# Kernel optimization log

Measured on AMD Instinct MI355X. Metric: run time of the kernel, lower is better.

## Reference

```python
import jax, jax.numpy as jnp
import numpy as np

EPS = 1e-6
SLIDING_WINDOW = 512
ROPE_BASE = 10000.0  # rope_local_base_freq for sliding_attention layers


def _rms_norm(x, w=None):
    # Gemma-style RMSNorm computed in fp32 then cast back
    xf = x.astype(jnp.float32)
    out = xf * jax.lax.rsqrt(jnp.mean(xf * xf, axis=-1, keepdims=True) + EPS)
    if w is not None:
        out = out * w.astype(jnp.float32)
    return out.astype(x.dtype)


def _rotate_half(x):
    x1, x2 = jnp.split(x, 2, axis=-1)
    return jnp.concatenate((-x2, x1), axis=-1)


def setup_inputs() -> dict:
    key = jax.random.key(0)
    ks = jax.random.split(key, 6)
    B, S, H, NH, NKV, D = 1, 4096, 2048, 8, 2, 256
    hidden_states = jax.random.normal(ks[0], (B, S, H), dtype=jnp.float32)
    w_q = jax.random.normal(ks[1], (H, NH * D), dtype=jnp.float32) * 0.02
    w_k = jax.random.normal(ks[2], (H, NKV * D), dtype=jnp.float32) * 0.02
    w_v = jax.random.normal(ks[3], (H, NKV * D), dtype=jnp.float32) * 0.02
    w_o = jax.random.normal(ks[4], (NH * D, H), dtype=jnp.float32) * 0.02
    q_norm_w = jnp.ones((D,), dtype=jnp.float32)
    k_norm_w = jnp.ones((D,), dtype=jnp.float32)
    # RoPE tables (local base freq, sliding layer)
    inv_freq = 1.0 / (ROPE_BASE ** (jnp.arange(0, D, 2, dtype=jnp.float32) / D))
    pos = jnp.arange(S, dtype=jnp.float32)
    freqs = pos[:, None] * inv_freq[None, :]          # [S, D/2]
    emb = jnp.concatenate((freqs, freqs), axis=-1)    # [S, D]
    cos = jnp.broadcast_to(jnp.cos(emb)[None], (B, S, D)).astype(jnp.float32)
    sin = jnp.broadcast_to(jnp.sin(emb)[None], (B, S, D)).astype(jnp.float32)
    return {"hidden_states": hidden_states, "w_q": w_q, "w_k": w_k, "w_v": w_v,
            "w_o": w_o, "q_norm_w": q_norm_w, "k_norm_w": k_norm_w,
            "cos": cos, "sin": sin}


def reference(hidden_states, w_q, w_k, w_v, w_o, q_norm_w, k_norm_w, cos, sin):
    B, S, _ = hidden_states.shape
    D = cos.shape[-1]
    NH = w_q.shape[1] // D
    NKV = w_k.shape[1] // D
    G = NH // NKV

    # projections -> [B, S, heads, D], per-head RMSNorm (Gemma3n-style)
    q = _rms_norm((hidden_states @ w_q).reshape(B, S, NH, D), q_norm_w)
    k = _rms_norm((hidden_states @ w_k).reshape(B, S, NKV, D), k_norm_w)
    v = _rms_norm((hidden_states @ w_v).reshape(B, S, NKV, D))  # v_norm: no scale

    q = q.transpose(0, 2, 1, 3)  # [B, NH, S, D]
    k = k.transpose(0, 2, 1, 3)  # [B, NKV, S, D]
    v = v.transpose(0, 2, 1, 3)

    # RoPE, cos/sin unsqueezed over the head dim
    c = cos[:, None, :, :]
    s = sin[:, None, :, :]
    q = q * c + _rotate_half(q) * s
    k = k * c + _rotate_half(k) * s

    # GQA: repeat KV heads
    k = jnp.repeat(k, G, axis=1)  # [B, NH, S, D]
    v = jnp.repeat(v, G, axis=1)

    # attention, scaling = 1.0 (q_norm replaces 1/sqrt(d) in this family)
    scores = jnp.einsum('bhqd,bhkd->bhqk', q, k)

    # causal + sliding-window mask
    i = jnp.arange(S)[:, None]
    j = jnp.arange(S)[None, :]
    mask = (j <= i) & ((i - j) < SLIDING_WINDOW)
    scores = jnp.where(mask[None, None], scores, jnp.finfo(scores.dtype).min)

    attn = jax.nn.softmax(scores.astype(jnp.float32), axis=-1).astype(q.dtype)
    out = jnp.einsum('bhqk,bhkd->bhqd', attn, v)
    out = out.transpose(0, 2, 1, 3).reshape(B, S, NH * D)
    return out @ w_o
```

## Files before the change

### kernel.cpp

```cpp
#include <hip/hip_runtime.h>
#include <hip/hip_bf16.h>

#define S_LEN 4096
#define HDIM  2048
#define NHQ   8
#define NKVH  2
#define DHEAD 256
#define WIN   512
#define NQKV  3072

typedef __hip_bfloat16 bf16_t;
using fragAB = __attribute__((ext_vector_type(8))) short;
using fragC  = __attribute__((ext_vector_type(4))) float;

struct __align__(8)  bf16x4 { bf16_t v[4]; };
struct __align__(16) bf16x8 { bf16_t v[8]; };

typedef unsigned int u32;
typedef const __attribute__((address_space(1))) u32* gas_ptr;
typedef __attribute__((address_space(3))) u32* las_ptr;

__device__ __forceinline__ void async_copy16(const void* g, void* l) {
  __builtin_amdgcn_global_load_lds((gas_ptr)g, (las_ptr)l, 16, 0, 0);
}

#define NEG_BIG (-3.0e38f)

__device__ __forceinline__ void split2(float x, bf16_t& hi, bf16_t& lo) {
  bf16_t h = __float2bfloat16(x);
  hi = h;
  lo = __float2bfloat16(x - (float)h);
}

__global__ __launch_bounds__(256) void prep0(
    const float* __restrict__ hid, bf16_t* __restrict__ hidh,
    bf16_t* __restrict__ hidl, const float* __restrict__ wq,
    const float* __restrict__ wk, const float* __restrict__ wv,
    bf16_t* __restrict__ hiT, bf16_t* __restrict__ loT) {
  __shared__ bf16_t th[32][33];
  __shared__ bf16_t tl[32][33];
  int bx = blockIdx.x;
  if (bx < 4096) {
    int i = (bx * 256 + threadIdx.x) * 8;
    float4 a = *(const float4*)(hid + i);
    float4 b = *(const float4*)(hid + i + 4);
    float xs[8] = {a.x, a.y, a.z, a.w, b.x, b.y, b.z, b.w};
    bf16x8 hv, lv;
#pragma unroll
    for (int j = 0; j < 8; ++j) split2(xs[j], hv.v[j], lv.v[j]);
    *(bf16x8*)(hidh + i) = hv;
    *(bf16x8*)(hidl + i) = lv;
  } else {
    int b2 = bx - 4096;
    int oc = (b2 % 96) * 32;
    int r0 = (b2 / 96) * 32;
    const float* src; int C, c0;
    if (oc < 2048)      { src = wq; C = 2048; c0 = oc; }
    else if (oc < 2560) { src = wk; C = 512;  c0 = oc - 2048; }
    else                { src = wv; C = 512;  c0 = oc - 2560; }
    int tx = threadIdx.x & 31, ty = threadIdx.x >> 5;
#pragma unroll
    for (int i = 0; i < 4; ++i) {
      float x = src[(size_t)(r0 + ty + i * 8) * C + c0 + tx];
      bf16_t h, l; split2(x, h, l);
      th[ty + i * 8][tx] = h;
      tl[ty + i * 8][tx] = l;
    }
    __syncthreads();
#pragma unroll
    for (int i = 0; i < 4; ++i) {
      hiT[(size_t)(oc + ty + i * 8) * HDIM + r0 + tx] = th[tx][ty + i * 8];
      loT[(size_t)(oc + ty + i * 8) * HDIM + r0 + tx] = tl[tx][ty + i * 8];
    }
  }
}

#define VMCNT_(n) asm volatile("s_waitcnt vmcnt(" #n ")" ::: "memory")
#define VMCNT(n) VMCNT_(n)
#define BARRIER()                     \
  {                                   \
    asm volatile("" ::: "memory");    \
    __builtin_amdgcn_s_barrier();     \
    asm volatile("" ::: "memory");    \
  }

#define MFMA_(a, b, c) __builtin_amdgcn_mfma_f32_16x16x32_bf16(a, b, c, 0, 0, 0)

#define OFF_AH 0
#define OFF_AL 16384
#define OFF_BH 32768
#define OFF_BL 45056
#define BUFSZ  57344

#define SPLIT_STEP()                                                    \
  {                                                                     \
    fragAB bh[4], bl[4];                                                \
    _Pragma("unroll") for (int j = 0; j < 4; ++j) {                     \
      const char* bp = bufc + (wn + j * 16 + l16) * 64 + rdq;           \
      bh[j] = *(const fragAB*)(bp + OFF_BH);                            \
      bl[j] = *(const fragAB*)(bp + OFF_BL);                            \
    }                                                                   \
    _Pragma("unroll") for (int p = 0; p < 2; ++p) {                     \
      fragAB ah[2], al[2];                                              \
      _Pragma("unroll") for (int u = 0; u < 2; ++u) {                   \
        const char* ap = bufc + (wm + (2 * p + u) * 16 + l16) * 64 + rdq;\
        ah[u] = *(const fragAB*)(ap + OFF_AH);                          \
        al[u] = *(const fragAB*)(ap + OFF_AL);                          \
      }                                                                 \
      __builtin_amdgcn_s_setprio(1);                                    \
      _Pragma("unroll") for (int j = 0; j < 4; ++j)                     \
        _Pragma("unroll") for (int u = 0; u < 2; ++u)                   \
          acc[2 * p + u][j] = MFMA_(al[u], bh[j], acc[2 * p + u][j]);   \
      _Pragma("unroll") for (int j = 0; j < 4; ++j)                     \
        _Pragma("unroll") for (int u = 0; u < 2; ++u)                   \
          acc[2 * p + u][j] = MFMA_(ah[u], bl[j], acc[2 * p + u][j]);   \
      _Pragma("unroll") for (int j = 0; j < 4; ++j)                     \
        _Pragma("unroll") for (int u = 0; u < 2; ++u)                   \
          acc[2 * p + u][j] = MFMA_(ah[u], bh[j], acc[2 * p + u][j]);   \
      __builtin_amdgcn_s_setprio(0);                                    \
    }                                                                   \
  }

__global__ __launch_bounds__(768, 3) void gemm_split2(
    const bf16_t* __restrict__ Ah, const bf16_t* __restrict__ Al,
    const bf16_t* __restrict__ Bh, const bf16_t* __restrict__ Bl,
    float* __restrict__ C, int M, int N, int K) {
  __shared__ __align__(16) char lds[2 * BUFSZ];
  const int t = threadIdx.x;
  const int wave = t >> 6, lane = t & 63;
  const int quad = lane >> 4, l16 = lane & 15;
  const int g = blockIdx.y * 16 + blockIdx.x;
  const int lby = (g & 7) * 2 + ((g >> 3) >> 4);
  const int lbx = (g >> 3) & 15;
  const int m0 = lby * 256, n0 = lbx * 192;
  const int wm = (wave / 3) * 64, wn = (wave % 3) * 64;
  const int rdq = (quad ^ ((l16 >> 1) & 3)) * 16;

  const size_t laneOff =
      (size_t)(lane >> 2) * K * 2 + 16 * ((lane & 3) ^ ((lane >> 3) & 3));

  const char* gbase[7];
  int ldsOff[7];
  if (wave < 8) {
#pragma unroll
    for (int pos = 0; pos < 3; ++pos) {
      int c = wave + 8 * pos;
      if (c < 12) {
        gbase[pos]  = (const char*)Bh + (size_t)(n0 + 16 * c) * K * 2;
        ldsOff[pos] = OFF_BH + c * 1024;
      } else {
        gbase[pos]  = (const char*)Bl + (size_t)(n0 + 16 * (c - 12)) * K * 2;
        ldsOff[pos] = OFF_BL + (c - 12) * 1024;
      }
    }
#pragma unroll
    for (int p = 0; p < 4; ++p) {
      int sub = wave & 3;
      int R0 = ((sub >> 1) & 1) * 128 + 32 * p + (sub & 1) * 16;
      const char* base = (const char*)(wave < 4 ? Ah : Al);
      gbase[3 + p]  = base + (size_t)(m0 + R0) * K * 2;
      ldsOff[3 + p] = (wave < 4 ? OFF_AH : OFF_AL) + R0 * 64;
    }
  }

  fragC zero4 = {0.f, 0.f, 0.f, 0.f};
  fragC acc[4][4];
#pragma unroll
  for (int i = 0; i < 4; ++i)
#pragma unroll
    for (int j = 0; j < 4; ++j) acc[i][j] = zero4;

  char* ldsc = (char*)lds;
  if (wave < 8) {
#pragma unroll
    for (int ps = 0; ps < 7; ++ps)
      async_copy16(gbase[ps] + laneOff, ldsc + ldsOff[ps]);
  }

  size_t kk = 64;
  int cur = 0;
  const int NS = K / 32;
  for (int it = 0; it < NS - 1; ++it) {
    const char* bufc = ldsc + cur * BUFSZ;
    char* nb = ldsc + (cur ^ 1) * BUFSZ;
    VMCNT(0); BARRIER();
    if (wave < 8) {
#pragma unroll
      for (int ps = 0; ps < 7; ++ps)
        async_copy16(gbase[ps] + kk + laneOff, nb + ldsOff[ps]);
    }
    kk += 64;
    SPLIT_STEP();
    cur ^= 1;
  }
  {
    const char* bufc = ldsc + cur * BUFSZ;
    VMCNT(0); BARRIER();
    SPLIT_STEP();
  }

#pragma unroll
  for (int i = 0; i < 4; ++i)
#pragma unroll
    for (int j = 0; j < 4; ++j)
#pragma unroll
      for (int r = 0; r < 4; ++r) {
        int row = m0 + wm + i * 16 + quad * 4 + r;
        int col = n0 + wn + j * 16 + l16;
        C[(size_t)row * N + col] = acc[i][j][r];
      }
}

#define BT_OFF_A 0
#define BT_OFF_B 32768
#define BT_BUFSZ 49152

struct ARegs2 { fragAB a[2][2]; };

__device__ __forceinline__ void lda_bt(ARegs2& r, const char* bufc, int wm,
                                       int p, int l16, int quad, int rx) {
#pragma unroll
  for (int u = 0; u < 2; ++u)
#pragma unroll
    for (int ks = 0; ks < 2; ++ks)
      r.a[u][ks] = *(const fragAB*)(bufc + BT_OFF_A +
                                    (wm + (2 * p + u) * 16 + l16) * 128 +
                                    (((ks * 4 + quad) ^ rx) * 16));
}

__device__ __forceinline__ void mfma_bt(fragC (&acc)[8][2], const ARegs2& r,
                                        const fragAB (&b)[2][2], int p) {
  __builtin_amdgcn_s_setprio(1);
#pragma unroll
  for (int ks = 0; ks < 2; ++ks)
#pragma unroll
    for (int j = 0; j < 2; ++j) {
      acc[2 * p][j]     = MFMA_(r.a[0][ks], b[j][ks], acc[2 * p][j]);
      acc[2 * p + 1][j] = MFMA_(r.a[1][ks], b[j][ks], acc[2 * p + 1][j]);
    }
  __builtin_amdgcn_s_setprio(0);
}

#define BT_LOADB()                                                        \
  _Pragma("unroll")                                                       \
  for (int j = 0; j < 2; ++j)                                             \
  _Pragma("unroll")                                                       \
    for (int ks = 0; ks < 2; ++ks)                                        \
      bfr[j][ks] = *(const fragAB*)(bufc + BT_OFF_B +                     \
                                    (wn + j * 16 + l16) * 128 +           \
                                    (((ks * 4 + quad) ^ rx) * 16));

#define BT_STEP()                                 \
  {                                               \
    BT_LOADB();                                   \
    lda_bt(r0, bufc, wm, 0, l16, quad, rx);       \
    lda_bt(r1, bufc, wm, 1, l16, quad, rx);       \
    mfma_bt(acc, r0, bfr, 0);                     \
    lda_bt(r0, bufc, wm, 2, l16, quad, rx);       \
    mfma_bt(acc, r1, bfr, 1);                     \
    lda_bt(r1, bufc, wm, 3, l16, quad, rx);       \
    mfma_bt(acc, r0, bfr, 2);                     \
    mfma_bt(acc, r1, bfr, 3);                     \
  }

__global__ __launch_bounds__(512, 2) void gemm_bt2(
    const bf16_t* __restrict__ A, const bf16_t* __restrict__ Bt,
    float* __restrict__ C, int M, int N, int K) {
  __shared__ __align__(16) char lds[2 * BT_BUFSZ];
  const int t = threadIdx.x;
  const int wave = t >> 6, lane = t & 63;
  const int quad = lane >> 4, l16 = lane & 15;
  const int g = blockIdx.y * 16 + blockIdx.x;
  const int lby = (g & 7) * 2 + ((g >> 3) >> 4);
  const int lbx = (g >> 3) & 15;
  const int m0 = lby * 256, n0 = lbx * 128;
  const int wm = (wave >> 2) * 128, wn = (wave & 3) * 32;
  const int rx = l16 & 7;

  const size_t laneOff =
      (size_t)(lane >> 3) * K * 2 + 16 * ((lane & 7) ^ ((lane >> 3) & 7));

  const char* gsrc[6];
  int ldsOff[6];
#pragma unroll
  for (int pos = 0; pos < 2; ++pos) {
    int c = wave + 8 * pos;
    gsrc[pos]   = (const char*)Bt + (size_t)(n0 + 8 * c) * K * 2 + laneOff;
    ldsOff[pos] = BT_OFF_B + c * 1024;
  }
#pragma unroll
  for (int p = 0; p < 4; ++p) {
    int R0 = (wave >> 2) * 128 + 32 * p + (wave & 3) * 8;
    gsrc[2 + p]   = (const char*)A + (size_t)(m0 + R0) * K * 2 + laneOff;
    ldsOff[2 + p] = BT_OFF_A + R0 * 128;
  }

  fragC zero4 = {0.f, 0.f, 0.f, 0.f};
  fragC acc[8][2];
#pragma unroll
  for (int i = 0; i < 8; ++i)
#pragma unroll
    for (int j = 0; j < 2; ++j) acc[i][j] = zero4;

  char* ldsc = (char*)lds;
#pragma unroll
  for (int ps = 0; ps < 6; ++ps) async_copy16(gsrc[ps], ldsc + ldsOff[ps]);
#pragma unroll
  for (int ps = 0; ps < 6; ++ps) gsrc[ps] += 128;

  fragAB bfr[2][2];
  ARegs2 r0, r1;
  int cur = 0;
  const int NS = K / 64;
  for (int it = 0; it < NS - 1; ++it) {
    const char* bufc = ldsc + cur * BT_BUFSZ;
    char* nb = ldsc + (cur ^ 1) * BT_BUFSZ;
    VMCNT(0); BARRIER();
#pragma unroll
    for (int ps = 0; ps < 6; ++ps) async_copy16(gsrc[ps], nb + ldsOff[ps]);
#pragma unroll
    for (int ps = 0; ps < 6; ++ps) gsrc[ps] += 128;
    BT_STEP();
    cur ^= 1;
  }
  {
    const char* bufc = ldsc + cur * BT_BUFSZ;
    VMCNT(0); BARRIER();
    BT_STEP();
  }

#pragma unroll
  for (int i = 0; i < 8; ++i)
#pragma unroll
    for (int j = 0; j < 2; ++j)
#pragma unroll
      for (int r = 0; r < 4; ++r) {
        int row = m0 + wm + i * 16 + quad * 4 + r;
        int col = n0 + wn + j * 16 + l16;
        C[(size_t)row * N + col] = acc[i][j][r];
      }
}

__global__ __launch_bounds__(256) void prep2(
    const float* __restrict__ proj, const float* __restrict__ qnw,
    const float* __restrict__ knw, const float* __restrict__ cosb,
    const float* __restrict__ sinb, bf16_t* __restrict__ qhi,
    bf16_t* __restrict__ qlo, bf16_t* __restrict__ khi,
    bf16_t* __restrict__ klo, bf16_t* __restrict__ vt,
    const float* __restrict__ wo, bf16_t* __restrict__ woT) {
  __shared__ float rs_[32];
  __shared__ bf16_t tile[32][33];
  int bx = blockIdx.x;
  if (bx < 10240) {
    const int wv = threadIdx.x >> 6, lane = threadIdx.x & 63;
    const int idx = bx * 4 + wv;
    const int s = idx / (NHQ + NKVH), hb = idx % (NHQ + NKVH);
    const float* w; bf16_t* oh; bf16_t* ol; int inOff, outStride, oBase;
    if (hb < NHQ) {
      w = qnw; oh = qhi; ol = qlo;
      inOff = hb * DHEAD; outStride = NHQ * DHEAD; oBase = hb * DHEAD;
    } else {
      int hk = hb - NHQ;
      w = knw; oh = khi; ol = klo;
      inOff = NHQ * DHEAD + hk * DHEAD; outStride = NKVH * DHEAD; oBase = hk * DHEAD;
    }
    const int d = lane * 4;
    float4 x = *(const float4*)(proj + (size_t)s * NQKV + inOff + d);
    float ss = x.x * x.x + x.y * x.y + x.z * x.z + x.w * x.w;
    ss += __shfl_xor(ss, 1);  ss += __shfl_xor(ss, 2);  ss += __shfl_xor(ss, 4);
    ss += __shfl_xor(ss, 8);  ss += __shfl_xor(ss, 16); ss += __shfl_xor(ss, 32);
    float r = rsqrtf(ss * (1.0f / DHEAD) + 1e-6f);
    float4 w4 = *(const float4*)(w + d);
    float xn[4] = {x.x * r * w4.x, x.y * r * w4.y, x.z * r * w4.z, x.w * r * w4.w};
    float ot[4];
#pragma unroll
    for (int j = 0; j < 4; ++j) ot[j] = __shfl_xor(xn[j], 32);
    float sgn = (lane < 32) ? -1.0f : 1.0f;
    float4 c4 = *(const float4*)(cosb + (size_t)s * DHEAD + d);
    float4 s4 = *(const float4*)(sinb + (size_t)s * DHEAD + d);
    float cc[4] = {c4.x, c4.y, c4.z, c4.w};
    float sn[4] = {s4.x, s4.y, s4.z, s4.w};
    bf16x4 hv, lv;
#pragma unroll
    for (int j = 0; j < 4; ++j) {
      float y = xn[j] * cc[j] + sgn * ot[j] * sn[j];
      split2(y, hv.v[j], lv.v[j]);
    }
    size_t o = (size_t)s * outStride + oBase + d;
    *(bf16x4*)(oh + o) = hv;
    *(bf16x4*)(ol + o) = lv;
  } else if (bx < 10240 + 256) {
    int b2 = bx - 10240;
    int s0 = (b2 & 127) * 32, hh = b2 >> 7;
    const int inOff = NHQ * DHEAD + NKVH * DHEAD;
    const float* base = proj + (size_t)s0 * NQKV + inOff + hh * DHEAD;
    int t = threadIdx.x;
    int sl = t >> 3, c8 = t & 7;
    const float4* rowp = (const float4*)(base + (size_t)sl * NQKV + c8 * 32);
    float ss = 0.f;
#pragma unroll
    for (int i = 0; i < 8; ++i) {
      float4 v = rowp[i];
      ss += v.x * v.x + v.y * v.y + v.z * v.z + v.w * v.w;
    }
    ss += __shfl_xor(ss, 1); ss += __shfl_xor(ss, 2); ss += __shfl_xor(ss, 4);
    if (c8 == 0) rs_[sl] = rsqrtf(ss * (1.0f / DHEAD) + 1e-6f);
    __syncthreads();
    int tx = t & 31, ty = t >> 5;
#pragma unroll
    for (int ch = 0; ch < 8; ++ch) {
#pragma unroll
      for (int i = 0; i < 4; ++i) {
        int s_ = ty + i * 8;
        float x = base[(size_t)s_ * NQKV + ch * 32 + tx];
        tile[s_][tx] = __float2bfloat16(x * rs_[s_]);
      }
      __syncthreads();
#pragma unroll
      for (int i = 0; i < 4; ++i) {
        int dl = ty + i * 8;
        vt[((size_t)hh * DHEAD + ch * 32 + dl) * S_LEN + s0 + tx] = tile[tx][dl];
      }
      __syncthreads();
    }
  } else {
    int b2 = bx - 10496;
    int c0 = (b2 & 63) * 32, r0 = (b2 >> 6) * 32;
    int tx = threadIdx.x & 31, ty = threadIdx.x >> 5;
#pragma unroll
    for (int i = 0; i < 4; ++i)
      tile[ty + i * 8][tx] =
          __float2bfloat16(wo[(size_t)(r0 + ty + i * 8) * HDIM + c0 + tx]);
    __syncthreads();
#pragma unroll
    for (int i = 0; i < 4; ++i)
      woT[(size_t)(c0 + ty + i * 8) * (NHQ * DHEAD) + r0 + tx] = tile[tx][ty + i * 8];
  }
}

__global__ __launch_bounds__(512, 2) void attn_split(
    const bf16_t* __restrict__ Qhi, const bf16_t* __restrict__ Qlo,
    const bf16_t* __restrict__ Khi, const bf16_t* __restrict__ Klo,
    const bf16_t* __restrict__ Vt, bf16_t* __restrict__ Aout) {
  const int g = blockIdx.y * 32 + blockIdx.x;
  const int lbx = (g & 7) * 4 + ((g >> 3) & 3);
  const int h = g >> 5;
  const int qb = lbx * 128;
  const int wave = threadIdx.x >> 6, lane = threadIdx.x & 63;
  const int quad = lane >> 4, l16 = lane & 15;
  const int qw = qb + wave * 16;
  const int kv = h >> 2;
  const bf16_t* Qh_ = Qhi + h * DHEAD;
  const bf16_t* Ql_ = Qlo + h * DHEAD;
  const bf16_t* Kh_ = Khi + kv * DHEAD;
  const bf16_t* Kl_ = Klo + kv * DHEAD;
  const bf16_t* Vh_ = Vt + (size_t)kv * DHEAD * S_LEN;

  __shared__ __align__(16) bf16_t KshH[2][32 * 256];
  __shared__ __align__(16) bf16_t KshL[2][32 * 256];
  __shared__ __align__(16) bf16_t Vsh[2][256 * 32];
  __shared__ __align__(16) bf16_t Plds[8][16 * 32];

  fragAB qfh[8], qfl[8];
#pragma unroll
  for (int c = 0; c < 8; ++c) {
    size_t off = (size_t)(qw + l16) * (NHQ * DHEAD) + c * 32 + quad * 8;
    qfh[c] = *(const fragAB*)(Qh_ + off);
    qfl[c] = *(const fragAB*)(Ql_ + off);
  }

  int kRow[2], kCol[2], vRow[2], vCol[2];
#pragma unroll
  for (int i = 0; i < 2; ++i) {
    int ci = i * 512 + threadIdx.x;
    kRow[i] = ci >> 5;
    kCol[i] = ((ci & 31) ^ (kRow[i] & 31)) * 8;
    vRow[i] = ci >> 2;
    vCol[i] = ((ci & 3) ^ (vRow[i] & 3)) * 8;
  }

#define ASTAGE(buf, kb_)                                                     \
  _Pragma("unroll")                                                          \
  for (int i = 0; i < 2; ++i) {                                              \
    size_t dst = (size_t)(i * 512 + threadIdx.x) * 16;                       \
    size_t koff = (size_t)((kb_) + kRow[i]) * (NKVH * DHEAD) + kCol[i];      \
    async_copy16(Kh_ + koff, (char*)KshH[buf] + dst);                        \
    async_copy16(Kl_ + koff, (char*)KshL[buf] + dst);                        \
    async_copy16(Vh_ + (size_t)vRow[i] * S_LEN + (kb_) + vCol[i],            \
                 (char*)Vsh[buf] + dst);                                     \
  }

  fragC zero4 = {0.f, 0.f, 0.f, 0.f};
  fragC o_acc[16];
#pragma unroll
  for (int c = 0; c < 16; ++c) o_acc[c] = zero4;
  float m_run[4] = {NEG_BIG, NEG_BIG, NEG_BIG, NEG_BIG};
  float l_run[4] = {0.f, 0.f, 0.f, 0.f};
  const float LOG2E = 1.4426950408889634f;

  int k_lo = qb - (WIN - 1);
  if (k_lo < 0) k_lo = 0;
  k_lo &= ~31;

  ASTAGE(0, k_lo);
  int cur = 0;

  for (int kb = k_lo; kb < qb + 128; kb += 32) {
    VMCNT(0); BARRIER();
    if (kb + 32 < qb + 128) {
      int nbuf = cur ^ 1;
      ASTAGE(nbuf, kb + 32);
    }
    const char* KH = (const char*)KshH[cur];
    const char* KL = (const char*)KshL[cur];
    const char* VB = (const char*)Vsh[cur];

    fragC s[2] = {zero4, zero4};
    __builtin_amdgcn_s_setprio(1);
#pragma unroll
    for (int c = 0; c < 8; ++c) {
      int j = c * 4 + quad;
#pragma unroll
      for (int gg = 0; gg < 2; ++gg) {
        int row = gg * 16 + l16;
        int off = (row * 32 + (j ^ (row & 31))) * 16;
        fragAB kh = *(const fragAB*)(KH + off);
        fragAB kl = *(const fragAB*)(KL + off);
        s[gg] = __builtin_amdgcn_mfma_f32_16x16x32_bf16(qfl[c], kh, s[gg], 0, 0, 0);
        s[gg] = __builtin_amdgcn_mfma_f32_16x16x32_bf16(qfh[c], kl, s[gg], 0, 0, 0);
        s[gg] = __builtin_amdgcn_mfma_f32_16x16x32_bf16(qfh[c], kh, s[gg], 0, 0, 0);
      }
    }
    __builtin_amdgcn_s_setprio(0);

    float p[2][4], alpha[4];
#pragma unroll
    for (int r = 0; r < 4; ++r) {
      int qi = qw + quad * 4 + r;
      bool vld[2];
      float mx = NEG_BIG;
#pragma unroll
      for (int gg = 0; gg < 2; ++gg) {
        int ki = kb + gg * 16 + l16;
        vld[gg] = (ki <= qi) && (qi - ki < WIN);
        mx = fmaxf(mx, vld[gg] ? s[gg][r] : NEG_BIG);
      }
      mx = fmaxf(mx, __shfl_xor(mx, 1));
      mx = fmaxf(mx, __shfl_xor(mx, 2));
      mx = fmaxf(mx, __shfl_xor(mx, 4));
      mx = fmaxf(mx, __shfl_xor(mx, 8));
      float mn = fmaxf(m_run[r], mx);
      float a  = exp2f(fmaxf(m_run[r] - mn, -80.f) * LOG2E);
      float rs = 0.f;
#pragma unroll
      for (int gg = 0; gg < 2; ++gg) {
        float e = vld[gg] ? exp2f(fmaxf(s[gg][r] - mn, -80.f) * LOG2E) : 0.f;
        p[gg][r] = e;
        rs += e;
      }
      rs += __shfl_xor(rs, 1);
      rs += __shfl_xor(rs, 2);
      rs += __shfl_xor(rs, 4);
      rs += __shfl_xor(rs, 8);
      l_run[r] = l_run[r] * a + rs;
      m_run[r] = mn;
      alpha[r] = a;
    }
#pragma unroll
    for (int c = 0; c < 16; ++c)
#pragma unroll
      for (int r = 0; r < 4; ++r) o_acc[c][r] *= alpha[r];

    bf16_t* Pw = Plds[wave];
#pragma unroll
    for (int r = 0; r < 4; ++r)
#pragma unroll
      for (int gg = 0; gg < 2; ++gg)
        Pw[(quad * 4 + r) * 32 + gg * 16 + l16] = __float2bfloat16(p[gg][r]);
    fragAB pf = *(const fragAB*)((const char*)Pw + l16 * 64 + quad * 16);

    __builtin_amdgcn_s_setprio(1);
#pragma unroll
    for (int c = 0; c < 16; ++c) {
      int d = c * 16 + l16;
      int offv = (d * 4 + (quad ^ (d & 3))) * 16;
      fragAB vf = *(const fragAB*)(VB + offv);
      o_acc[c] = __builtin_amdgcn_mfma_f32_16x16x32_bf16(pf, vf, o_acc[c], 0, 0, 0);
    }
    __builtin_amdgcn_s_setprio(0);
    cur ^= 1;
  }

  float inv_l[4];
#pragma unroll
  for (int r = 0; r < 4; ++r) inv_l[r] = 1.0f / l_run[r];
#pragma unroll
  for (int c = 0; c < 16; ++c)
#pragma unroll
    for (int r = 0; r < 4; ++r) {
      int row = qw + quad * 4 + r;
      int col = h * DHEAD + c * 16 + l16;
      Aout[(size_t)row * (NHQ * DHEAD) + col] = __float2bfloat16(o_acc[c][r] * inv_l[r]);
    }
#undef ASTAGE
}

extern "C" void kernel_launch(void* const* d_in, const int* in_sizes, int n_in,
                              void* d_out, int out_size, void* d_ws, size_t ws_size,
                              hipStream_t stream) {
  const float* hid  = (const float*)d_in[0];
  const float* w_q  = (const float*)d_in[1];
  const float* w_k  = (const float*)d_in[2];
  const float* w_v  = (const float*)d_in[3];
  const float* w_o  = (const float*)d_in[4];
  const float* qnw  = (const float*)d_in[5];
  const float* knw  = (const float*)d_in[6];
  const float* cosb = (const float*)d_in[7];
  const float* sinb = (const float*)d_in[8];
  float* outp = (float*)d_out;

  const size_t M1 = 1048576;
  bf16_t* w = (bf16_t*)d_ws;
  bf16_t* hidh  = w;
  bf16_t* qh    = w;
  bf16_t* hidl  = w + 8 * M1;
  bf16_t* ql    = w + 8 * M1;
  bf16_t* wTh   = w + 16 * M1;
  bf16_t* kh    = w + 16 * M1;
  bf16_t* kl    = w + 18 * M1;
  bf16_t* vt    = w + 20 * M1;
  bf16_t* wTl   = w + 22 * M1;
  bf16_t* woT   = w + 22 * M1;
  float*  projqkv = (float*)(w + 28 * M1);
  bf16_t* aout  = w + 28 * M1;

  prep0<<<4096 + 96 * 64, 256, 0, stream>>>(
      hid, hidh, hidl, w_q, w_k, w_v, wTh, wTl);

  gemm_split2<<<dim3(NQKV / 192, S_LEN / 256), 768, 0, stream>>>(
      hidh, hidl, wTh, wTl, projqkv, S_LEN, NQKV, HDIM);

  prep2<<<10240 + 256 + 4096, 256, 0, stream>>>(
      projqkv, qnw, knw, cosb, sinb, qh, ql, kh, kl, vt, w_o, woT);

  attn_split<<<dim3(S_LEN / 128, NHQ), 512, 0, stream>>>(qh, ql, kh, kl, vt, aout);

  gemm_bt2<<<dim3(HDIM / 128, S_LEN / 256), 512, 0, stream>>>(
      aout, woT, outp, S_LEN, HDIM, NHQ * DHEAD);
}
```

Measured before the change: 393.0 us.

## Use 16 waves per block in both GEMMs with smaller per-wave tiles

```diff
diff --git a/kernel.cpp b/kernel.cpp
--- a/kernel.cpp
+++ b/kernel.cpp
@@ -94,8 +94,8 @@
 
 #define SPLIT_STEP()                                                    \
   {                                                                     \
-    fragAB bh[4], bl[4];                                                \
-    _Pragma("unroll") for (int j = 0; j < 4; ++j) {                     \
+    fragAB bh[3], bl[3];                                                \
+    _Pragma("unroll") for (int j = 0; j < 3; ++j) {                     \
       const char* bp = bufc + (wn + j * 16 + l16) * 64 + rdq;           \
       bh[j] = *(const fragAB*)(bp + OFF_BH);                            \
       bl[j] = *(const fragAB*)(bp + OFF_BL);                            \
@@ -108,20 +108,20 @@
         al[u] = *(const fragAB*)(ap + OFF_AL);                          \
       }                                                                 \
       __builtin_amdgcn_s_setprio(1);                                    \
-      _Pragma("unroll") for (int j = 0; j < 4; ++j)                     \
+      _Pragma("unroll") for (int j = 0; j < 3; ++j)                     \
         _Pragma("unroll") for (int u = 0; u < 2; ++u)                   \
           acc[2 * p + u][j] = MFMA_(al[u], bh[j], acc[2 * p + u][j]);   \
-      _Pragma("unroll") for (int j = 0; j < 4; ++j)                     \
+      _Pragma("unroll") for (int j = 0; j < 3; ++j)                     \
         _Pragma("unroll") for (int u = 0; u < 2; ++u)                   \
           acc[2 * p + u][j] = MFMA_(ah[u], bl[j], acc[2 * p + u][j]);   \
-      _Pragma("unroll") for (int j = 0; j < 4; ++j)                     \
+      _Pragma("unroll") for (int j = 0; j < 3; ++j)                     \
         _Pragma("unroll") for (int u = 0; u < 2; ++u)                   \
           acc[2 * p + u][j] = MFMA_(ah[u], bh[j], acc[2 * p + u][j]);   \
       __builtin_amdgcn_s_setprio(0);                                    \
     }                                                                   \
   }
 
-__global__ __launch_bounds__(768, 3) void gemm_split2(
+__global__ __launch_bounds__(1024, 4) void gemm_split2(
     const bf16_t* __restrict__ Ah, const bf16_t* __restrict__ Al,
     const bf16_t* __restrict__ Bh, const bf16_t* __restrict__ Bl,
     float* __restrict__ C, int M, int N, int K) {
@@ -133,49 +133,37 @@
   const int lby = (g & 7) * 2 + ((g >> 3) >> 4);
   const int lbx = (g >> 3) & 15;
   const int m0 = lby * 256, n0 = lbx * 192;
-  const int wm = (wave / 3) * 64, wn = (wave % 3) * 64;
+  const int wm = (wave >> 2) * 64, wn = (wave & 3) * 48;
   const int rdq = (quad ^ ((l16 >> 1) & 3)) * 16;
 
   const size_t laneOff =
       (size_t)(lane >> 2) * K * 2 + 16 * ((lane & 3) ^ ((lane >> 3) & 3));
 
-  const char* gbase[7];
-  int ldsOff[7];
-  if (wave < 8) {
-#pragma unroll
-    for (int pos = 0; pos < 3; ++pos) {
-      int c = wave + 8 * pos;
-      if (c < 12) {
-        gbase[pos]  = (const char*)Bh + (size_t)(n0 + 16 * c) * K * 2;
-        ldsOff[pos] = OFF_BH + c * 1024;
-      } else {
-        gbase[pos]  = (const char*)Bl + (size_t)(n0 + 16 * (c - 12)) * K * 2;
-        ldsOff[pos] = OFF_BL + (c - 12) * 1024;
-      }
-    }
-#pragma unroll
-    for (int p = 0; p < 4; ++p) {
-      int sub = wave & 3;
-      int R0 = ((sub >> 1) & 1) * 128 + 32 * p + (sub & 1) * 16;
-      const char* base = (const char*)(wave < 4 ? Ah : Al);
-      gbase[3 + p]  = base + (size_t)(m0 + R0) * K * 2;
-      ldsOff[3 + p] = (wave < 4 ? OFF_AH : OFF_AL) + R0 * 64;
-    }
+  const char* gbase[4];
+  int ldsOff[4];
+  const int nch = (wave < 8) ? 4 : 3;
+#pragma unroll
+  for (int pos = 0; pos < 4; ++pos) {
+    int c = (pos < 3) ? (wave + 16 * pos) : (48 + wave);
+    const char* gb; int lo;
+    if (c < 12)      { gb = (const char*)Bh + (size_t)(n0 + 16 * c) * K * 2;        lo = OFF_BH + c * 1024; }
+    else if (c < 24) { gb = (const char*)Bl + (size_t)(n0 + 16 * (c - 12)) * K * 2; lo = OFF_BL + (c - 12) * 1024; }
+    else if (c < 40) { gb = (const char*)Ah + (size_t)(m0 + 16 * (c - 24)) * K * 2; lo = OFF_AH + (c - 24) * 1024; }
+    else             { gb = (const char*)Al + (size_t)(m0 + 16 * (c - 40)) * K * 2; lo = OFF_AL + (c - 40) * 1024; }
+    gbase[pos] = gb;
+    ldsOff[pos] = lo;
   }
 
   fragC zero4 = {0.f, 0.f, 0.f, 0.f};
-  fragC acc[4][4];
+  fragC acc[4][3];
 #pragma unroll
   for (int i = 0; i < 4; ++i)
 #pragma unroll
-    for (int j = 0; j < 4; ++j) acc[i][j] = zero4;
+    for (int j = 0; j < 3; ++j) acc[i][j] = zero4;
 
   char* ldsc = (char*)lds;
-  if (wave < 8) {
-#pragma unroll
-    for (int ps = 0; ps < 7; ++ps)
-      async_copy16(gbase[ps] + laneOff, ldsc + ldsOff[ps]);
-  }
+  for (int ps = 0; ps < nch; ++ps)
+    async_copy16(gbase[ps] + laneOff, ldsc + ldsOff[ps]);
 
   size_t kk = 64;
   int cur = 0;
@@ -184,11 +172,8 @@
     const char* bufc = ldsc + cur * BUFSZ;
     char* nb = ldsc + (cur ^ 1) * BUFSZ;
     VMCNT(0); BARRIER();
-    if (wave < 8) {
-#pragma unroll
-      for (int ps = 0; ps < 7; ++ps)
-        async_copy16(gbase[ps] + kk + laneOff, nb + ldsOff[ps]);
-    }
+    for (int ps = 0; ps < nch; ++ps)
+      async_copy16(gbase[ps] + kk + laneOff, nb + ldsOff[ps]);
     kk += 64;
     SPLIT_STEP();
     cur ^= 1;
@@ -202,7 +187,7 @@
 #pragma unroll
   for (int i = 0; i < 4; ++i)
 #pragma unroll
-    for (int j = 0; j < 4; ++j)
+    for (int j = 0; j < 3; ++j)
 #pragma unroll
       for (int r = 0; r < 4; ++r) {
         int row = m0 + wm + i * 16 + quad * 4 + r;
@@ -215,55 +200,31 @@
 #define BT_OFF_B 32768
 #define BT_BUFSZ 49152
 
-struct ARegs2 { fragAB a[2][2]; };
-
-__device__ __forceinline__ void lda_bt(ARegs2& r, const char* bufc, int wm,
-                                       int p, int l16, int quad, int rx) {
-#pragma unroll
-  for (int u = 0; u < 2; ++u)
-#pragma unroll
-    for (int ks = 0; ks < 2; ++ks)
-      r.a[u][ks] = *(const fragAB*)(bufc + BT_OFF_A +
-                                    (wm + (2 * p + u) * 16 + l16) * 128 +
-                                    (((ks * 4 + quad) ^ rx) * 16));
-}
-
-__device__ __forceinline__ void mfma_bt(fragC (&acc)[8][2], const ARegs2& r,
-                                        const fragAB (&b)[2][2], int p) {
-  __builtin_amdgcn_s_setprio(1);
-#pragma unroll
-  for (int ks = 0; ks < 2; ++ks)
-#pragma unroll
-    for (int j = 0; j < 2; ++j) {
-      acc[2 * p][j]     = MFMA_(r.a[0][ks], b[j][ks], acc[2 * p][j]);
-      acc[2 * p + 1][j] = MFMA_(r.a[1][ks], b[j][ks], acc[2 * p + 1][j]);
-    }
-  __builtin_amdgcn_s_setprio(0);
-}
-
-#define BT_LOADB()                                                        \
-  _Pragma("unroll")                                                       \
-  for (int j = 0; j < 2; ++j)                                             \
-  _Pragma("unroll")                                                       \
-    for (int ks = 0; ks < 2; ++ks)                                        \
-      bfr[j][ks] = *(const fragAB*)(bufc + BT_OFF_B +                     \
-                                    (wn + j * 16 + l16) * 128 +           \
-                                    (((ks * 4 + quad) ^ rx) * 16));
-
-#define BT_STEP()                                 \
-  {                                               \
-    BT_LOADB();                                   \
-    lda_bt(r0, bufc, wm, 0, l16, quad, rx);       \
-    lda_bt(r1, bufc, wm, 1, l16, quad, rx);       \
-    mfma_bt(acc, r0, bfr, 0);                     \
-    lda_bt(r0, bufc, wm, 2, l16, quad, rx);       \
-    mfma_bt(acc, r1, bfr, 1);                     \
-    lda_bt(r1, bufc, wm, 3, l16, quad, rx);       \
-    mfma_bt(acc, r0, bfr, 2);                     \
-    mfma_bt(acc, r1, bfr, 3);                     \
-  }
-
-__global__ __launch_bounds__(512, 2) void gemm_bt2(
+#define BT_STEP()                                                         \
+  {                                                                       \
+    fragAB bfr[2][2];                                                     \
+    _Pragma("unroll") for (int j = 0; j < 2; ++j)                         \
+      _Pragma("unroll") for (int ks = 0; ks < 2; ++ks)                    \
+        bfr[j][ks] = *(const fragAB*)(bufc + BT_OFF_B +                   \
+                                      (wn + j * 16 + l16) * 128 +         \
+                                      (((ks * 4 + quad) ^ rx) * 16));     \
+    _Pragma("unroll") for (int p = 0; p < 2; ++p) {                       \
+      fragAB af[2][2];                                                    \
+      _Pragma("unroll") for (int u = 0; u < 2; ++u)                       \
+        _Pragma("unroll") for (int ks = 0; ks < 2; ++ks)                  \
+          af[u][ks] = *(const fragAB*)(bufc + BT_OFF_A +                  \
+                                       (wm + (2 * p + u) * 16 + l16) * 128 + \
+                                       (((ks * 4 + quad) ^ rx) * 16));    \
+      __builtin_amdgcn_s_setprio(1);                                      \
+      _Pragma("unroll") for (int ks = 0; ks < 2; ++ks)                    \
+        _Pragma("unroll") for (int j = 0; j < 2; ++j)                     \
+          _Pragma("unroll") for (int u = 0; u < 2; ++u)                   \
+            acc[2 * p + u][j] = MFMA_(af[u][ks], bfr[j][ks], acc[2 * p + u][j]); \
+      __builtin_amdgcn_s_setprio(0);                                      \
+    }                                                                     \
+  }
+
+__global__ __launch_bounds__(1024, 4) void gemm_bt2(
     const bf16_t* __restrict__ A, const bf16_t* __restrict__ Bt,
     float* __restrict__ C, int M, int N, int K) {
   __shared__ __align__(16) char lds[2 * BT_BUFSZ];
@@ -274,42 +235,39 @@
   const int lby = (g & 7) * 2 + ((g >> 3) >> 4);
   const int lbx = (g >> 3) & 15;
   const int m0 = lby * 256, n0 = lbx * 128;
-  const int wm = (wave >> 2) * 128, wn = (wave & 3) * 32;
+  const int wm = (wave >> 2) * 64, wn = (wave & 3) * 32;
   const int rx = l16 & 7;
 
   const size_t laneOff =
       (size_t)(lane >> 3) * K * 2 + 16 * ((lane & 7) ^ ((lane >> 3) & 7));
 
-  const char* gsrc[6];
-  int ldsOff[6];
-#pragma unroll
-  for (int pos = 0; pos < 2; ++pos) {
-    int c = wave + 8 * pos;
-    gsrc[pos]   = (const char*)Bt + (size_t)(n0 + 8 * c) * K * 2 + laneOff;
-    ldsOff[pos] = BT_OFF_B + c * 1024;
-  }
-#pragma unroll
-  for (int p = 0; p < 4; ++p) {
-    int R0 = (wave >> 2) * 128 + 32 * p + (wave & 3) * 8;
-    gsrc[2 + p]   = (const char*)A + (size_t)(m0 + R0) * K * 2 + laneOff;
-    ldsOff[2 + p] = BT_OFF_A + R0 * 128;
+  const char* gbase[3];
+  int ldsOff[3];
+#pragma unroll
+  for (int pos = 0; pos < 3; ++pos) {
+    int c = wave + 16 * pos;
+    if (c < 16) {
+      gbase[pos]  = (const char*)Bt + (size_t)(n0 + 8 * c) * K * 2;
+      ldsOff[pos] = BT_OFF_B + c * 1024;
+    } else {
+      gbase[pos]  = (const char*)A + (size_t)(m0 + 8 * (c - 16)) * K * 2;
+      ldsOff[pos] = BT_OFF_A + (c - 16) * 1024;
+    }
   }
 
   fragC zero4 = {0.f, 0.f, 0.f, 0.f};
-  fragC acc[8][2];
-#pragma unroll
-  for (int i = 0; i < 8; ++i)
+  fragC acc[4][2];
+#pragma unroll
+  for (int i = 0; i < 4; ++i)
 #pragma unroll
     for (int j = 0; j < 2; ++j) acc[i][j] = zero4;
 
   char* ldsc = (char*)lds;
 #pragma unroll
-  for (int ps = 0; ps < 6; ++ps) async_copy16(gsrc[ps], ldsc + ldsOff[ps]);
-#pragma unroll
-  for (int ps = 0; ps < 6; ++ps) gsrc[ps] += 128;
-
-  fragAB bfr[2][2];
-  ARegs2 r0, r1;
+  for (int ps = 0; ps < 3; ++ps)
+    async_copy16(gbase[ps] + laneOff, ldsc + ldsOff[ps]);
+
+  size_t kk = 128;
   int cur = 0;
   const int NS = K / 64;
   for (int it = 0; it < NS - 1; ++it) {
@@ -317,9 +275,9 @@
     char* nb = ldsc + (cur ^ 1) * BT_BUFSZ;
     VMCNT(0); BARRIER();
 #pragma unroll
-    for (int ps = 0; ps < 6; ++ps) async_copy16(gsrc[ps], nb + ldsOff[ps]);
-#pragma unroll
-    for (int ps = 0; ps < 6; ++ps) gsrc[ps] += 128;
+    for (int ps = 0; ps < 3; ++ps)
+      async_copy16(gbase[ps] + kk + laneOff, nb + ldsOff[ps]);
+    kk += 128;
     BT_STEP();
     cur ^= 1;
   }
@@ -330,7 +288,7 @@
   }
 
 #pragma unroll
-  for (int i = 0; i < 8; ++i)
+  for (int i = 0; i < 4; ++i)
 #pragma unroll
     for (int j = 0; j < 2; ++j)
 #pragma unroll
@@ -637,7 +595,7 @@
   prep0<<<4096 + 96 * 64, 256, 0, stream>>>(
       hid, hidh, hidl, w_q, w_k, w_v, wTh, wTl);
 
-  gemm_split2<<<dim3(NQKV / 192, S_LEN / 256), 768, 0, stream>>>(
+  gemm_split2<<<dim3(NQKV / 192, S_LEN / 256), 1024, 0, stream>>>(
       hidh, hidl, wTh, wTl, projqkv, S_LEN, NQKV, HDIM);
 
   prep2<<<10240 + 256 + 4096, 256, 0, stream>>>(
@@ -645,6 +603,6 @@
 
   attn_split<<<dim3(S_LEN / 128, NHQ), 512, 0, stream>>>(qh, ql, kh, kl, vt, aout);
 
-  gemm_bt2<<<dim3(HDIM / 128, S_LEN / 256), 512, 0, stream>>>(
+  gemm_bt2<<<dim3(HDIM / 128, S_LEN / 256), 1024, 0, stream>>>(
       aout, woT, outp, S_LEN, HDIM, NHQ * DHEAD);
 }
```

Result: no change. 396.0 us (+0.8%).
